# Kernel optimization log

Hardware: AMD Instinct MI355X
Metric: run time of the kernel (lower is better)

Reference implementation:

```python
import jax, jax.numpy as jnp
import numpy as np

IN_FEATURES = 512
OUT_FEATURES = 512
BATCH = 1024


def setup_inputs() -> dict:
    key = jax.random.key(0)
    k_x, k_bw, k_ww, k_sc, k_tr, k_b = jax.random.split(key, 6)
    std = 1.0 / np.sqrt(IN_FEATURES)
    x = jax.random.normal(k_x, (BATCH, IN_FEATURES), dtype=jnp.float32)
    base_weight = jax.random.uniform(k_bw, (OUT_FEATURES, IN_FEATURES), jnp.float32, -std, std)
    wavelet_weights = jax.random.uniform(k_ww, (OUT_FEATURES, IN_FEATURES), jnp.float32, -std, std)
    # scale initialized to ones in the module; perturb slightly (kept positive) for a non-degenerate test
    scale = jnp.exp(0.1 * jax.random.normal(k_sc, (OUT_FEATURES, IN_FEATURES), dtype=jnp.float32))
    translation = 0.1 * jax.random.normal(k_tr, (OUT_FEATURES, IN_FEATURES), dtype=jnp.float32)
    bias = jax.random.uniform(k_b, (OUT_FEATURES,), jnp.float32, -std, std)
    return {"x": x, "base_weight": base_weight, "wavelet_weights": wavelet_weights,
            "scale": scale, "translation": translation, "bias": bias}


def reference(x, base_weight, wavelet_weights, scale, translation, bias):
    # base branch: SiLU then linear
    base_out = jnp.einsum("bi,oi->bo", jax.nn.silu(x), base_weight)
    # wavelet branch: broadcast x to (batch, out, in)
    xs = (x[:, None, :] - translation[None, :, :]) / scale[None, :, :]  # (B, O, I)
    wavelet = (xs * xs - 1.0) * jnp.exp(-0.5 * xs * xs)  # mexican hat
    wavelet_out = jnp.einsum("boi,oi->bo", wavelet, wavelet_weights)
    return base_out + wavelet_out + bias
```

## Files before the change

### kernel.cpp

```cpp
#include <hip/hip_runtime.h>


constexpr int IN_F  = 512;
constexpr int OUT_F = 512;
constexpr int BATCH = 1024;
constexpr int BT = 64, OT = 64;
constexpr int KS = 8;
constexpr int KR = IN_F / KS;
constexpr int IT = 16;
constexpr int PITCH = IT + 4;
constexpr int NCH = KR / IT;
constexpr int BO  = BATCH * OUT_F;

#define LOG2E 1.44269504088897f
#define C2f   (-0.72134752044448f)
#define NC2f  ( 0.72134752044448f)
#define RQf   (-0.84083003f)

typedef float v2f __attribute__((ext_vector_type(2)));

__device__ __forceinline__ float fexp2(float v) { return __builtin_amdgcn_exp2f(v); }
__device__ __forceinline__ float frcp(float v)  { return __builtin_amdgcn_rcpf(v); }
__device__ __forceinline__ v2f pkfma(v2f a, v2f b, v2f c) {
  return __builtin_elementwise_fma(a, b, c);
}
__device__ __forceinline__ float fsilu(float v) {
  return v * frcp(1.f + fexp2(v * -LOG2E));
}

__global__ __launch_bounds__(256, 4)
void wkan_main(const float* __restrict__ x, const float* __restrict__ basew,
               const float* __restrict__ wavew, const float* __restrict__ scale,
               const float* __restrict__ transl, const float* __restrict__ bias,
               float* __restrict__ partial, float* __restrict__ out, int use_ws)
{
  __shared__ float lx [BT * PITCH];
  __shared__ float lsx[BT * PITCH];
  __shared__ float la [OT * PITCH];
  __shared__ float lm [OT * PITCH];
  __shared__ float ln [OT * PITCH];
  __shared__ float lq [OT * PITCH];
  __shared__ float lb [OT * PITCH];

  const int tid = threadIdx.x;
  const int b0 = blockIdx.x * BT;
  const int o0 = blockIdx.y * OT;
  const int ks = blockIdx.z;
  const int k0 = ks * KR;

  const int srow = tid >> 2;
  const int sc4  = (tid & 3) * 4;
  const int lofs = srow * PITCH + sc4;

  const int to = tid & 15;
  const int tb = tid >> 4;

  v2f zz; zz.x = 0.f; zz.y = 0.f;
  v2f acc[4][4];
#pragma unroll
  for (int r = 0; r < 4; ++r)
#pragma unroll
    for (int c = 0; c < 4; ++c) acc[r][c] = zz;

  for (int kc = 0; kc < NCH; ++kc) {
    const int g = k0 + kc * IT + sc4;
    __syncthreads();
    {
      float4 xv = *(const float4*)(x + (size_t)(b0 + srow) * IN_F + g);
      float4 sx;
      sx.x = fsilu(xv.x); sx.y = fsilu(xv.y); sx.z = fsilu(xv.z); sx.w = fsilu(xv.w);
      *(float4*)(lx  + lofs) = xv;
      *(float4*)(lsx + lofs) = sx;

      float4 sv = *(const float4*)(scale  + (size_t)(o0 + srow) * IN_F + g);
      float4 tv = *(const float4*)(transl + (size_t)(o0 + srow) * IN_F + g);
      float4 av, mv, nv;
      {
        float a2, a2t;
        a2 = C2f * frcp(sv.x * sv.x); a2t = a2 * tv.x;
        av.x = a2; mv.x = -2.f * a2t; nv.x = fmaf(a2t, tv.x, NC2f);
        a2 = C2f * frcp(sv.y * sv.y); a2t = a2 * tv.y;
        av.y = a2; mv.y = -2.f * a2t; nv.y = fmaf(a2t, tv.y, NC2f);
        a2 = C2f * frcp(sv.z * sv.z); a2t = a2 * tv.z;
        av.z = a2; mv.z = -2.f * a2t; nv.z = fmaf(a2t, tv.z, NC2f);
        a2 = C2f * frcp(sv.w * sv.w); a2t = a2 * tv.w;
        av.w = a2; mv.w = -2.f * a2t; nv.w = fmaf(a2t, tv.w, NC2f);
      }
      *(float4*)(la + lofs) = av;
      *(float4*)(lm + lofs) = mv;
      *(float4*)(ln + lofs) = nv;

      float4 wv = *(const float4*)(wavew + (size_t)(o0 + srow) * IN_F + g);
      float4 qv;
      qv.x = wv.x * RQf; qv.y = wv.y * RQf; qv.z = wv.z * RQf; qv.w = wv.w * RQf;
      *(float4*)(lq + lofs) = qv;

      float4 bv = *(const float4*)(basew + (size_t)(o0 + srow) * IN_F + g);
      *(float4*)(lb + lofs) = bv;
    }
    __syncthreads();

    for (int ii = 0; ii < IT; ii += 4) {
      float4 xr[4], sr[4], x2[4];
#pragma unroll
      for (int r = 0; r < 4; ++r) {
        const int row = (tb + 16 * r) * PITCH + ii;
        xr[r] = *(const float4*)(lx + row);
        sr[r] = *(const float4*)(lsx + row);
        x2[r].x = xr[r].x * xr[r].x;
        x2[r].y = xr[r].y * xr[r].y;
        x2[r].z = xr[r].z * xr[r].z;
        x2[r].w = xr[r].w * xr[r].w;
      }
#pragma unroll
      for (int c = 0; c < 4; ++c) {
        const int orow = (to + 16 * c) * PITCH + ii;
        float4 A = *(const float4*)(la + orow);
        float4 M = *(const float4*)(lm + orow);
        float4 N = *(const float4*)(ln + orow);
        float4 Q = *(const float4*)(lq + orow);
        float4 B = *(const float4*)(lb + orow);
        v2f Al = {A.x, A.y}, Ah = {A.z, A.w};
        v2f Ml = {M.x, M.y}, Mh = {M.z, M.w};
        v2f Nl = {N.x, N.y}, Nh = {N.z, N.w};
        v2f Ql = {Q.x, Q.y}, Qh = {Q.z, Q.w};
        v2f Bl = {B.x, B.y}, Bh = {B.z, B.w};
#pragma unroll
        for (int r = 0; r < 4; ++r) {
          v2f xl  = {xr[r].x, xr[r].y}, xh  = {xr[r].z, xr[r].w};
          v2f x2l = {x2[r].x, x2[r].y}, x2h = {x2[r].z, x2[r].w};
          v2f sl  = {sr[r].x, sr[r].y}, sh  = {sr[r].z, sr[r].w};
          v2f p, e, gg;
          p = pkfma(Al, x2l, pkfma(Ml, xl, Nl));
          e.x = fexp2(p.x); e.y = fexp2(p.y);
          gg = p * Ql;
          acc[r][c] = pkfma(gg, e, acc[r][c]);
          acc[r][c] = pkfma(sl, Bl, acc[r][c]);
          p = pkfma(Ah, x2h, pkfma(Mh, xh, Nh));
          e.x = fexp2(p.x); e.y = fexp2(p.y);
          gg = p * Qh;
          acc[r][c] = pkfma(gg, e, acc[r][c]);
          acc[r][c] = pkfma(sh, Bh, acc[r][c]);
        }
      }
    }
  }

#pragma unroll
  for (int r = 0; r < 4; ++r) {
    const int br = b0 + tb + 16 * r;
#pragma unroll
    for (int c = 0; c < 4; ++c) {
      const int oc = o0 + to + 16 * c;
      float res = acc[r][c].x + acc[r][c].y;
      if (use_ws) {
        partial[(size_t)ks * BO + (size_t)br * OUT_F + oc] = res;
      } else {
        if (ks == 0) res += bias[oc];
        atomicAdd(out + (size_t)br * OUT_F + oc, res);
      }
    }
  }
}

__global__ __launch_bounds__(256)
void wkan_reduce(const float* __restrict__ partial, const float* __restrict__ bias,
                 float* __restrict__ out)
{
  const int i4 = (blockIdx.x * 256 + threadIdx.x) * 4;
  float4 r = *(const float4*)(bias + (i4 & (OUT_F - 1)));
#pragma unroll
  for (int k = 0; k < KS; ++k) {
    float4 a = *(const float4*)(partial + (size_t)k * BO + i4);
    r.x += a.x; r.y += a.y; r.z += a.z; r.w += a.w;
  }
  *(float4*)(out + i4) = r;
}

extern "C" void kernel_launch(void* const* d_in, const int* in_sizes, int n_in,
                              void* d_out, int out_size, void* d_ws, size_t ws_size,
                              hipStream_t stream) {
  const float* x  = (const float*)d_in[0];
  const float* bw = (const float*)d_in[1];
  const float* ww = (const float*)d_in[2];
  const float* sc = (const float*)d_in[3];
  const float* tr = (const float*)d_in[4];
  const float* bi = (const float*)d_in[5];
  float* out = (float*)d_out;

  const int use_ws = ws_size >= (size_t)KS * BO * sizeof(float) ? 1 : 0;
  if (!use_ws) {
    hipMemsetAsync(d_out, 0, (size_t)out_size * sizeof(float), stream);
  }
  dim3 grid(BATCH / BT, OUT_F / OT, KS);
  wkan_main<<<grid, dim3(256), 0, stream>>>(x, bw, ww, sc, tr, bi,
                                            (float*)d_ws, out, use_ws);
  if (use_ws) {
    wkan_reduce<<<dim3(BO / 1024), dim3(256), 0, stream>>>((const float*)d_ws, bi, out);
  }
}
```

Measured before the change: 113.4 us.

## Split SiLU base branch into separate bf16 MFMA GEMM kernel

Removes the SiLU base-weight term from the fused wavelet loop and computes it in a separate kernel using 16x16x32 bf16 MFMA, writing bias-added results into the output. The wavelet kernel drops two LDS arrays and one FMA per element, and its occupancy hint rises from 4 to 6 blocks. The reduce kernel now accumulates onto the GEMM output instead of the bias. This adds a kernel launch and lowers the base branch to bf16 precision, which could affect accuracy.

```diff
diff --git a/kernel.cpp b/kernel.cpp
--- a/kernel.cpp
+++ b/kernel.cpp
@@ -17,7 +17,9 @@
 #define NC2f  ( 0.72134752044448f)
 #define RQf   (-0.84083003f)
 
-typedef float v2f __attribute__((ext_vector_type(2)));
+typedef float v2f   __attribute__((ext_vector_type(2)));
+typedef float f32x4 __attribute__((ext_vector_type(4)));
+typedef short short8 __attribute__((ext_vector_type(8)));
 
 __device__ __forceinline__ float fexp2(float v) { return __builtin_amdgcn_exp2f(v); }
 __device__ __forceinline__ float frcp(float v)  { return __builtin_amdgcn_rcpf(v); }
@@ -27,20 +29,22 @@
 __device__ __forceinline__ float fsilu(float v) {
   return v * frcp(1.f + fexp2(v * -LOG2E));
 }
-
-__global__ __launch_bounds__(256, 4)
-void wkan_main(const float* __restrict__ x, const float* __restrict__ basew,
+__device__ __forceinline__ short bf16rne(float f) {
+  unsigned u = __float_as_uint(f);
+  return (short)((u + 0x7FFFu + ((u >> 16) & 1u)) >> 16);
+}
+
+__global__ __launch_bounds__(256, 6)
+void wkan_main(const float* __restrict__ x,
                const float* __restrict__ wavew, const float* __restrict__ scale,
-               const float* __restrict__ transl, const float* __restrict__ bias,
+               const float* __restrict__ transl,
                float* __restrict__ partial, float* __restrict__ out, int use_ws)
 {
   __shared__ float lx [BT * PITCH];
-  __shared__ float lsx[BT * PITCH];
   __shared__ float la [OT * PITCH];
   __shared__ float lm [OT * PITCH];
   __shared__ float ln [OT * PITCH];
   __shared__ float lq [OT * PITCH];
-  __shared__ float lb [OT * PITCH];
 
   const int tid = threadIdx.x;
   const int b0 = blockIdx.x * BT;
@@ -67,10 +71,7 @@
     __syncthreads();
     {
       float4 xv = *(const float4*)(x + (size_t)(b0 + srow) * IN_F + g);
-      float4 sx;
-      sx.x = fsilu(xv.x); sx.y = fsilu(xv.y); sx.z = fsilu(xv.z); sx.w = fsilu(xv.w);
-      *(float4*)(lx  + lofs) = xv;
-      *(float4*)(lsx + lofs) = sx;
+      *(float4*)(lx + lofs) = xv;
 
       float4 sv = *(const float4*)(scale  + (size_t)(o0 + srow) * IN_F + g);
       float4 tv = *(const float4*)(transl + (size_t)(o0 + srow) * IN_F + g);
@@ -94,19 +95,15 @@
       float4 qv;
       qv.x = wv.x * RQf; qv.y = wv.y * RQf; qv.z = wv.z * RQf; qv.w = wv.w * RQf;
       *(float4*)(lq + lofs) = qv;
-
-      float4 bv = *(const float4*)(basew + (size_t)(o0 + srow) * IN_F + g);
-      *(float4*)(lb + lofs) = bv;
     }
     __syncthreads();
 
     for (int ii = 0; ii < IT; ii += 4) {
-      float4 xr[4], sr[4], x2[4];
+      float4 xr[4], x2[4];
 #pragma unroll
       for (int r = 0; r < 4; ++r) {
         const int row = (tb + 16 * r) * PITCH + ii;
         xr[r] = *(const float4*)(lx + row);
-        sr[r] = *(const float4*)(lsx + row);
         x2[r].x = xr[r].x * xr[r].x;
         x2[r].y = xr[r].y * xr[r].y;
         x2[r].z = xr[r].z * xr[r].z;
@@ -119,28 +116,23 @@
         float4 M = *(const float4*)(lm + orow);
         float4 N = *(const float4*)(ln + orow);
         float4 Q = *(const float4*)(lq + orow);
-        float4 B = *(const float4*)(lb + orow);
         v2f Al = {A.x, A.y}, Ah = {A.z, A.w};
         v2f Ml = {M.x, M.y}, Mh = {M.z, M.w};
         v2f Nl = {N.x, N.y}, Nh = {N.z, N.w};
         v2f Ql = {Q.x, Q.y}, Qh = {Q.z, Q.w};
-        v2f Bl = {B.x, B.y}, Bh = {B.z, B.w};
 #pragma unroll
         for (int r = 0; r < 4; ++r) {
           v2f xl  = {xr[r].x, xr[r].y}, xh  = {xr[r].z, xr[r].w};
           v2f x2l = {x2[r].x, x2[r].y}, x2h = {x2[r].z, x2[r].w};
-          v2f sl  = {sr[r].x, sr[r].y}, sh  = {sr[r].z, sr[r].w};
           v2f p, e, gg;
           p = pkfma(Al, x2l, pkfma(Ml, xl, Nl));
           e.x = fexp2(p.x); e.y = fexp2(p.y);
           gg = p * Ql;
           acc[r][c] = pkfma(gg, e, acc[r][c]);
-          acc[r][c] = pkfma(sl, Bl, acc[r][c]);
           p = pkfma(Ah, x2h, pkfma(Mh, xh, Nh));
           e.x = fexp2(p.x); e.y = fexp2(p.y);
           gg = p * Qh;
           acc[r][c] = pkfma(gg, e, acc[r][c]);
-          acc[r][c] = pkfma(sh, Bh, acc[r][c]);
         }
       }
     }
@@ -156,19 +148,55 @@
       if (use_ws) {
         partial[(size_t)ks * BO + (size_t)br * OUT_F + oc] = res;
       } else {
-        if (ks == 0) res += bias[oc];
         atomicAdd(out + (size_t)br * OUT_F + oc, res);
       }
     }
   }
 }
 
+__global__ __launch_bounds__(64)
+void base_gemm(const float* __restrict__ x, const float* __restrict__ basew,
+               const float* __restrict__ bias, float* __restrict__ out)
+{
+  const int lane = threadIdx.x;
+  const int li  = lane & 15;
+  const int quad = lane >> 4;
+  const int bm = blockIdx.x * 16;
+  const int bn = blockIdx.y * 16;
+
+  const float* arow = x     + (size_t)(bm + li) * IN_F + quad * 8;
+  const float* brow = basew + (size_t)(bn + li) * IN_F + quad * 8;
+
+  f32x4 acc = {0.f, 0.f, 0.f, 0.f};
+  for (int k0 = 0; k0 < IN_F; k0 += 32) {
+    float4 a0 = *(const float4*)(arow + k0);
+    float4 a1 = *(const float4*)(arow + k0 + 4);
+    float4 b0 = *(const float4*)(brow + k0);
+    float4 b1 = *(const float4*)(brow + k0 + 4);
+    short8 af, bfv;
+    af[0] = bf16rne(fsilu(a0.x)); af[1] = bf16rne(fsilu(a0.y));
+    af[2] = bf16rne(fsilu(a0.z)); af[3] = bf16rne(fsilu(a0.w));
+    af[4] = bf16rne(fsilu(a1.x)); af[5] = bf16rne(fsilu(a1.y));
+    af[6] = bf16rne(fsilu(a1.z)); af[7] = bf16rne(fsilu(a1.w));
+    bfv[0] = bf16rne(b0.x); bfv[1] = bf16rne(b0.y);
+    bfv[2] = bf16rne(b0.z); bfv[3] = bf16rne(b0.w);
+    bfv[4] = bf16rne(b1.x); bfv[5] = bf16rne(b1.y);
+    bfv[6] = bf16rne(b1.z); bfv[7] = bf16rne(b1.w);
+    acc = __builtin_amdgcn_mfma_f32_16x16x32_bf16(af, bfv, acc, 0, 0, 0);
+  }
+  const float bi = bias[bn + li];
+#pragma unroll
+  for (int reg = 0; reg < 4; ++reg) {
+    const int row = quad * 4 + reg;
+    out[(size_t)(bm + row) * OUT_F + bn + li] = acc[reg] + bi;
+  }
+}
+
 __global__ __launch_bounds__(256)
-void wkan_reduce(const float* __restrict__ partial, const float* __restrict__ bias,
-                 float* __restrict__ out)
+void wkan_reduce(const float* __restrict__ partial, float* __restrict__ out)
 {
   const int i4 = (blockIdx.x * 256 + threadIdx.x) * 4;
-  float4 r = *(const float4*)(bias + (i4 & (OUT_F - 1)));
+  float4 r = *(const float4*)(out + i4);
 #pragma unroll
   for (int k = 0; k < KS; ++k) {
     float4 a = *(const float4*)(partial + (size_t)k * BO + i4);
@@ -189,13 +217,13 @@
   float* out = (float*)d_out;
 
   const int use_ws = ws_size >= (size_t)KS * BO * sizeof(float) ? 1 : 0;
-  if (!use_ws) {
-    hipMemsetAsync(d_out, 0, (size_t)out_size * sizeof(float), stream);
-  }
+
+  base_gemm<<<dim3(BATCH / 16, OUT_F / 16), dim3(64), 0, stream>>>(x, bw, bi, out);
+
   dim3 grid(BATCH / BT, OUT_F / OT, KS);
-  wkan_main<<<grid, dim3(256), 0, stream>>>(x, bw, ww, sc, tr, bi,
+  wkan_main<<<grid, dim3(256), 0, stream>>>(x, ww, sc, tr,
                                             (float*)d_ws, out, use_ws);
   if (use_ws) {
-    wkan_reduce<<<dim3(BO / 1024), dim3(256), 0, stream>>>((const float*)d_ws, bi, out);
-  }
-}
+    wkan_reduce<<<dim3(BO / 1024), dim3(256), 0, stream>>>((const float*)d_ws, out);
+  }
+}
```

New measurement: 271.9 us. 2.4x slower.
